# Kernel optimization log

Measured on AMD Instinct MI355X. Metric: run time of the kernel, lower is better.

The kernel has to match this reference:

```python
import jax, jax.numpy as jnp
import numpy as np

LOG2 = float(np.log(2.0))

def _ssp(x):
    # shifted softplus: softplus(x) - log(2)
    return jax.nn.softplus(x) - LOG2

def setup_inputs() -> dict:
    key = jax.random.key(0)
    ks = jax.random.split(key, 6)
    B, At, Nbr, F = 16, 512, 64, 128
    H = F // 2
    return {
        "last_edge_embedding": jax.random.normal(ks[0], (B, At, Nbr, F), dtype=jnp.float32),
        "unit_vecs": jax.random.normal(ks[1], (B, At, Nbr, 3), dtype=jnp.float32),
        "W1": jax.random.normal(ks[2], (F, H), dtype=jnp.float32) * (1.0 / np.sqrt(F)),
        "b1": jax.random.normal(ks[3], (H,), dtype=jnp.float32) * 0.01,
        "W2": jax.random.normal(ks[4], (H, 1), dtype=jnp.float32) * (1.0 / np.sqrt(H)),
        "b2": jax.random.normal(ks[5], (1,), dtype=jnp.float32) * 0.01,
    }

def reference(last_edge_embedding, unit_vecs, W1, b1, W2, b2):
    # Dense(F -> F/2) with shifted softplus activation
    h = _ssp(jnp.einsum('banf,fh->banh', last_edge_embedding, W1) + b1)
    # Dense(F/2 -> 1), no activation: per-edge force magnitude (B, At, Nbr, 1)
    force_magnitude = jnp.einsum('banh,ho->bano', h, W2) + b2
    # broadcast-multiply by unit vectors and sum over neighbor axis -> (B, At, 3)
    return (force_magnitude * unit_vecs).sum(axis=2)
```

## Files before the change

### kernel.cpp

```cpp
#include <hip/hip_runtime.h>


typedef __attribute__((ext_vector_type(8))) short short8;
typedef __attribute__((ext_vector_type(4))) float f32x4;

__device__ __forceinline__ unsigned bf16rn(float f) {
    unsigned u = __float_as_uint(f);
    unsigned r = 0x7FFFu + ((u >> 16) & 1u);
    return (u + r) >> 16;
}
__device__ __forceinline__ unsigned pack2(float lo, float hi) {
    return bf16rn(lo) | (bf16rn(hi) << 16);
}

__global__ void wfrag_kernel(const float* __restrict__ W1, unsigned* __restrict__ tab) {
    int t = blockIdx.x * blockDim.x + threadIdx.x;
    int frag = t >> 6, lane = t & 63;
    int kk = frag >> 2, nn = frag & 3;
    int q = lane >> 4, c = lane & 15;
    int n = nn * 16 + c;
    int k0 = kk * 32 + q * 8;
    unsigned w[4];
#pragma unroll
    for (int p = 0; p < 4; ++p) {
        float lo = W1[(k0 + 2 * p    ) * 64 + n];
        float hi = W1[(k0 + 2 * p + 1) * 64 + n];
        w[p] = pack2(lo, hi);
    }
    unsigned* dst = tab + (frag * 64 + lane) * 4;
    *(uint4*)dst = make_uint4(w[0], w[1], w[2], w[3]);
}

#define ATOMS_PER_BLOCK 4

__global__ __launch_bounds__(256, 4) void force_kernel(
    const float* __restrict__ emb,
    const float* __restrict__ uvec,
    const float* __restrict__ b1,
    const float* __restrict__ W2,
    const float* __restrict__ b2,
    const uint4* __restrict__ tab,
    float* __restrict__ out)
{
    const int tid  = threadIdx.x;
    const int wave = tid >> 6;
    const int lane = tid & 63;
    const int q = lane >> 4;
    const int c = lane & 15;

    __shared__ uint4 tab_lds[1024];
    __shared__ float red[ATOMS_PER_BLOCK][4][3];
#pragma unroll
    for (int i = 0; i < 4; ++i) tab_lds[i * 256 + tid] = tab[i * 256 + tid];
    __syncthreads();
    const short8* bfl = (const short8*)tab_lds;

    float b1v[4], w2v[4];
#pragma unroll
    for (int nn = 0; nn < 4; ++nn) {
        b1v[nn] = b1[nn * 16 + c];
        w2v[nn] = W2[nn * 16 + c];
    }
    const float b2v = b2[0];

    const int atom0 = blockIdx.x * ATOMS_PER_BLOCK;

    for (int ai = 0; ai < ATOMS_PER_BLOCK; ++ai) {
        const int ebase = (atom0 + ai) * 64 + wave * 16;

        float uv[4];
        if (c < 3) {
            const float* up = uvec + (ebase + q * 4) * 3 + c;
#pragma unroll
            for (int r = 0; r < 4; ++r) uv[r] = up[r * 3];
        }

        const float* aptr = emb + (ebase + c) * 128 + q * 8;
        float4 p[8];
#pragma unroll
        for (int kk = 0; kk < 4; ++kk) {
            p[2 * kk]     = *(const float4*)(aptr + kk * 32);
            p[2 * kk + 1] = *(const float4*)(aptr + kk * 32 + 4);
        }
        short8 afrag[4];
#pragma unroll
        for (int kk = 0; kk < 4; ++kk) {
            union { short8 s; unsigned u[4]; } cv;
            cv.u[0] = pack2(p[2 * kk].x,     p[2 * kk].y);
            cv.u[1] = pack2(p[2 * kk].z,     p[2 * kk].w);
            cv.u[2] = pack2(p[2 * kk + 1].x, p[2 * kk + 1].y);
            cv.u[3] = pack2(p[2 * kk + 1].z, p[2 * kk + 1].w);
            afrag[kk] = cv.s;
        }

        f32x4 acc[4] = {{0.f,0.f,0.f,0.f},{0.f,0.f,0.f,0.f},{0.f,0.f,0.f,0.f},{0.f,0.f,0.f,0.f}};
#pragma unroll
        for (int kk = 0; kk < 4; ++kk)
#pragma unroll
            for (int nn = 0; nn < 4; ++nn)
                acc[nn] = __builtin_amdgcn_mfma_f32_16x16x32_bf16(
                    afrag[kk], bfl[(kk * 4 + nn) * 64 + lane], acc[nn], 0, 0, 0);

        float fm[4];
#pragma unroll
        for (int r = 0; r < 4; ++r) {
            float s = 0.f;
#pragma unroll
            for (int nn = 0; nn < 4; ++nn) {
                float z  = acc[nn][r] + b1v[nn];
                float sp = fmaxf(z, 0.f) + __logf(1.f + __expf(-fabsf(z))) - 0.69314718056f;
                s += sp * w2v[nn];
            }
            fm[r] = s;
        }
#pragma unroll
        for (int m = 1; m < 16; m <<= 1) {
#pragma unroll
            for (int r = 0; r < 4; ++r) fm[r] += __shfl_xor(fm[r], m, 64);
        }

        float s = 0.f;
        if (c < 3) {
#pragma unroll
            for (int r = 0; r < 4; ++r) s += (fm[r] + b2v) * uv[r];
        }
        s += __shfl_xor(s, 16, 64);
        s += __shfl_xor(s, 32, 64);
        if (lane < 3) red[ai][wave][lane] = s;
    }

    __syncthreads();
    if (tid < ATOMS_PER_BLOCK * 3) {
        int ai = tid / 3, x = tid % 3;
        out[(atom0 + ai) * 3 + x] =
            red[ai][0][x] + red[ai][1][x] + red[ai][2][x] + red[ai][3][x];
    }
}

extern "C" void kernel_launch(void* const* d_in, const int* in_sizes, int n_in,
                              void* d_out, int out_size, void* d_ws, size_t ws_size,
                              hipStream_t stream) {
    const float* emb  = (const float*)d_in[0];
    const float* uvec = (const float*)d_in[1];
    const float* W1   = (const float*)d_in[2];
    const float* b1   = (const float*)d_in[3];
    const float* W2   = (const float*)d_in[4];
    const float* b2   = (const float*)d_in[5];
    float* out = (float*)d_out;

    unsigned* tab = (unsigned*)d_ws;

    wfrag_kernel<<<4, 256, 0, stream>>>(W1, tab);

    const int atoms = 16 * 512;
    force_kernel<<<atoms / ATOMS_PER_BLOCK, 256, 0, stream>>>(
        emb, uvec, b1, W2, b2, (const uint4*)tab, out);
}
```

Measured before the change: 371.1 us.

## Fuse weight-fragment prep into force kernel with one atom per block

Drops the separate W1 bf16 fragment kernel and has every block build the LDS weight table itself straight from W1. Each block now handles a single atom, and its embedding and unit-vector loads are issued before the table build and barrier so they overlap with it. This removes a kernel launch and adds memory-level parallelism through many more, smaller blocks. The cost is that every block redoes the W1 conversion, reading 32KB of W1 through the cache, with no loop over atoms to spread that cost.

```diff
diff --git a/kernel.cpp b/kernel.cpp
--- a/kernel.cpp
+++ b/kernel.cpp
@@ -13,33 +13,13 @@
     return bf16rn(lo) | (bf16rn(hi) << 16);
 }
 
-__global__ void wfrag_kernel(const float* __restrict__ W1, unsigned* __restrict__ tab) {
-    int t = blockIdx.x * blockDim.x + threadIdx.x;
-    int frag = t >> 6, lane = t & 63;
-    int kk = frag >> 2, nn = frag & 3;
-    int q = lane >> 4, c = lane & 15;
-    int n = nn * 16 + c;
-    int k0 = kk * 32 + q * 8;
-    unsigned w[4];
-#pragma unroll
-    for (int p = 0; p < 4; ++p) {
-        float lo = W1[(k0 + 2 * p    ) * 64 + n];
-        float hi = W1[(k0 + 2 * p + 1) * 64 + n];
-        w[p] = pack2(lo, hi);
-    }
-    unsigned* dst = tab + (frag * 64 + lane) * 4;
-    *(uint4*)dst = make_uint4(w[0], w[1], w[2], w[3]);
-}
-
-#define ATOMS_PER_BLOCK 4
-
 __global__ __launch_bounds__(256, 4) void force_kernel(
     const float* __restrict__ emb,
     const float* __restrict__ uvec,
+    const float* __restrict__ W1,
     const float* __restrict__ b1,
     const float* __restrict__ W2,
     const float* __restrict__ b2,
-    const uint4* __restrict__ tab,
     float* __restrict__ out)
 {
     const int tid  = threadIdx.x;
@@ -47,14 +27,39 @@
     const int lane = tid & 63;
     const int q = lane >> 4;
     const int c = lane & 15;
+    const int atom  = blockIdx.x;
+    const int ebase = atom * 64 + wave * 16;
 
-    __shared__ uint4 tab_lds[1024];
-    __shared__ float red[ATOMS_PER_BLOCK][4][3];
+    __shared__ uint4 tab[1024];
+    __shared__ float red[4][3];
+
+    const float* aptr = emb + (ebase + c) * 128 + q * 8;
+    float4 p[8];
 #pragma unroll
-    for (int i = 0; i < 4; ++i) tab_lds[i * 256 + tid] = tab[i * 256 + tid];
-    __syncthreads();
-    const short8* bfl = (const short8*)tab_lds;
+    for (int kk = 0; kk < 4; ++kk) {
+        p[2 * kk]     = *(const float4*)(aptr + kk * 32);
+        p[2 * kk + 1] = *(const float4*)(aptr + kk * 32 + 4);
+    }
+    float uv[4];
+    if (c < 3) {
+        const float* up = uvec + (ebase + q * 4) * 3 + c;
+#pragma unroll
+        for (int r = 0; r < 4; ++r) uv[r] = up[r * 3];
+    }
 
+#pragma unroll
+    for (int t = 0; t < 4; ++t) {
+        const int frag = wave * 4 + t;
+        const int kk = frag >> 2, nn = frag & 3;
+        const int k0 = kk * 32 + q * 8;
+        const int n  = nn * 16 + c;
+        uint4 w;
+        w.x = pack2(W1[(k0 + 0) * 64 + n], W1[(k0 + 1) * 64 + n]);
+        w.y = pack2(W1[(k0 + 2) * 64 + n], W1[(k0 + 3) * 64 + n]);
+        w.z = pack2(W1[(k0 + 4) * 64 + n], W1[(k0 + 5) * 64 + n]);
+        w.w = pack2(W1[(k0 + 6) * 64 + n], W1[(k0 + 7) * 64 + n]);
+        tab[frag * 64 + lane] = w;
+    }
     float b1v[4], w2v[4];
 #pragma unroll
     for (int nn = 0; nn < 4; ++nn) {
@@ -62,79 +67,58 @@
         w2v[nn] = W2[nn * 16 + c];
     }
     const float b2v = b2[0];
+    __syncthreads();
+    const short8* bfl = (const short8*)tab;
 
-    const int atom0 = blockIdx.x * ATOMS_PER_BLOCK;
-
-    for (int ai = 0; ai < ATOMS_PER_BLOCK; ++ai) {
-        const int ebase = (atom0 + ai) * 64 + wave * 16;
-
-        float uv[4];
-        if (c < 3) {
-            const float* up = uvec + (ebase + q * 4) * 3 + c;
+    short8 afrag[4];
 #pragma unroll
-            for (int r = 0; r < 4; ++r) uv[r] = up[r * 3];
-        }
-
-        const float* aptr = emb + (ebase + c) * 128 + q * 8;
-        float4 p[8];
-#pragma unroll
-        for (int kk = 0; kk < 4; ++kk) {
-            p[2 * kk]     = *(const float4*)(aptr + kk * 32);
-            p[2 * kk + 1] = *(const float4*)(aptr + kk * 32 + 4);
-        }
-        short8 afrag[4];
-#pragma unroll
-        for (int kk = 0; kk < 4; ++kk) {
-            union { short8 s; unsigned u[4]; } cv;
-            cv.u[0] = pack2(p[2 * kk].x,     p[2 * kk].y);
-            cv.u[1] = pack2(p[2 * kk].z,     p[2 * kk].w);
-            cv.u[2] = pack2(p[2 * kk + 1].x, p[2 * kk + 1].y);
-            cv.u[3] = pack2(p[2 * kk + 1].z, p[2 * kk + 1].w);
-            afrag[kk] = cv.s;
-        }
-
-        f32x4 acc[4] = {{0.f,0.f,0.f,0.f},{0.f,0.f,0.f,0.f},{0.f,0.f,0.f,0.f},{0.f,0.f,0.f,0.f}};
-#pragma unroll
-        for (int kk = 0; kk < 4; ++kk)
-#pragma unroll
-            for (int nn = 0; nn < 4; ++nn)
-                acc[nn] = __builtin_amdgcn_mfma_f32_16x16x32_bf16(
-                    afrag[kk], bfl[(kk * 4 + nn) * 64 + lane], acc[nn], 0, 0, 0);
-
-        float fm[4];
-#pragma unroll
-        for (int r = 0; r < 4; ++r) {
-            float s = 0.f;
-#pragma unroll
-            for (int nn = 0; nn < 4; ++nn) {
-                float z  = acc[nn][r] + b1v[nn];
-                float sp = fmaxf(z, 0.f) + __logf(1.f + __expf(-fabsf(z))) - 0.69314718056f;
-                s += sp * w2v[nn];
-            }
-            fm[r] = s;
-        }
-#pragma unroll
-        for (int m = 1; m < 16; m <<= 1) {
-#pragma unroll
-            for (int r = 0; r < 4; ++r) fm[r] += __shfl_xor(fm[r], m, 64);
-        }
-
-        float s = 0.f;
-        if (c < 3) {
-#pragma unroll
-            for (int r = 0; r < 4; ++r) s += (fm[r] + b2v) * uv[r];
-        }
-        s += __shfl_xor(s, 16, 64);
-        s += __shfl_xor(s, 32, 64);
-        if (lane < 3) red[ai][wave][lane] = s;
+    for (int kk = 0; kk < 4; ++kk) {
+        union { short8 s; unsigned u[4]; } cv;
+        cv.u[0] = pack2(p[2 * kk].x,     p[2 * kk].y);
+        cv.u[1] = pack2(p[2 * kk].z,     p[2 * kk].w);
+        cv.u[2] = pack2(p[2 * kk + 1].x, p[2 * kk + 1].y);
+        cv.u[3] = pack2(p[2 * kk + 1].z, p[2 * kk + 1].w);
+        afrag[kk] = cv.s;
     }
 
+    f32x4 acc[4] = {{0.f,0.f,0.f,0.f},{0.f,0.f,0.f,0.f},{0.f,0.f,0.f,0.f},{0.f,0.f,0.f,0.f}};
+#pragma unroll
+    for (int kk = 0; kk < 4; ++kk)
+#pragma unroll
+        for (int nn = 0; nn < 4; ++nn)
+            acc[nn] = __builtin_amdgcn_mfma_f32_16x16x32_bf16(
+                afrag[kk], bfl[(kk * 4 + nn) * 64 + lane], acc[nn], 0, 0, 0);
+
+    float fm[4];
+#pragma unroll
+    for (int r = 0; r < 4; ++r) {
+        float s = 0.f;
+#pragma unroll
+        for (int nn = 0; nn < 4; ++nn) {
+            float z  = acc[nn][r] + b1v[nn];
+            float sp = fmaxf(z, 0.f) + __logf(1.f + __expf(-fabsf(z))) - 0.69314718056f;
+            s += sp * w2v[nn];
+        }
+        fm[r] = s;
+    }
+#pragma unroll
+    for (int m = 1; m < 16; m <<= 1) {
+#pragma unroll
+        for (int r = 0; r < 4; ++r) fm[r] += __shfl_xor(fm[r], m, 64);
+    }
+
+    float s = 0.f;
+    if (c < 3) {
+#pragma unroll
+        for (int r = 0; r < 4; ++r) s += (fm[r] + b2v) * uv[r];
+    }
+    s += __shfl_xor(s, 16, 64);
+    s += __shfl_xor(s, 32, 64);
+    if (lane < 3) red[wave][lane] = s;
+
     __syncthreads();
-    if (tid < ATOMS_PER_BLOCK * 3) {
-        int ai = tid / 3, x = tid % 3;
-        out[(atom0 + ai) * 3 + x] =
-            red[ai][0][x] + red[ai][1][x] + red[ai][2][x] + red[ai][3][x];
-    }
+    if (tid < 3)
+        out[atom * 3 + tid] = red[0][tid] + red[1][tid] + red[2][tid] + red[3][tid];
 }
 
 extern "C" void kernel_launch(void* const* d_in, const int* in_sizes, int n_in,
@@ -148,11 +132,6 @@
     const float* b2   = (const float*)d_in[5];
     float* out = (float*)d_out;
 
-    unsigned* tab = (unsigned*)d_ws;
-
-    wfrag_kernel<<<4, 256, 0, stream>>>(W1, tab);
-
     const int atoms = 16 * 512;
-    force_kernel<<<atoms / ATOMS_PER_BLOCK, 256, 0, stream>>>(
-        emb, uvec, b1, W2, b2, (const uint4*)tab, out);
+    force_kernel<<<atoms, 256, 0, stream>>>(emb, uvec, W1, b1, W2, b2, out);
 }
```

Result: no change. 364.6 us (-1.7%).
